# Kernel optimization log

Hardware: AMD Instinct MI355X
Metric: run time of the kernel (lower is better)

## Reference

```python
import jax, jax.numpy as jnp
import numpy as np

N = 1_500_000  # nodes (250k tracklets x 6 hits)
E = 12_000_000  # edges


def setup_inputs() -> dict:
    key = jax.random.key(0)
    ks = jax.random.split(key, 26)
    w = lambda k, shape: (jax.random.normal(k, shape, jnp.float32) * 0.1)
    inp = {
        "x": jax.random.normal(ks[0], (N, 1), jnp.float32),
        "edge_index": jax.random.randint(ks[1], (2, E), 0, N),
        "edge_attr": jax.random.normal(ks[2], (E, 2), jnp.float32),
        # conv1: in=1, prop=9, edge=2, out=9
        "Wx1": w(ks[3], (9, 1)), "bx1": w(ks[4], (9,)),
        "We1": w(ks[5], (9, 2)), "be1": w(ks[6], (9,)),
        "Wo1": w(ks[7], (9, 9)), "bo1": w(ks[8], (9,)),
        # conv2: in=9, prop=9, edge=2, out=9
        "Wx2": w(ks[9], (9, 9)), "bx2": w(ks[10], (9,)),
        "We2": w(ks[11], (9, 2)), "be2": w(ks[12], (9,)),
        "Wo2": w(ks[13], (9, 9)), "bo2": w(ks[14], (9,)),
        # conv3: in=9, prop=9, edge=2, out=4
        "Wx3": w(ks[15], (9, 9)), "bx3": w(ks[16], (9,)),
        "We3": w(ks[17], (9, 2)), "be3": w(ks[18], (9,)),
        "Wo3": w(ks[19], (4, 9)), "bo3": w(ks[20], (4,)),
        # head MLP
        "W1": w(ks[21], (8, 24)), "b1": w(ks[22], (8,)),
        "W2": w(ks[23], (4, 8)), "b2": w(ks[24], (4,)),
    }
    return inp


def _conv(x, src, dst, edge_attr, Wx, bx, We, be, Wo, bo):
    # trackletGNN: lin_x -> gather x_j -> * lin_edge(edge_attr) -> scatter-add -> lin_out
    h = x @ Wx.T + bx                      # [N, P]
    msg = h[src] * (edge_attr @ We.T + be)  # [E, P] gather + edge linear + multiply
    agg = jax.ops.segment_sum(msg, dst, num_segments=x.shape[0])  # [N, P]
    return agg @ Wo.T + bo


def reference(x, edge_index, edge_attr,
              Wx1, bx1, We1, be1, Wo1, bo1,
              Wx2, bx2, We2, be2, Wo2, bo2,
              Wx3, bx3, We3, be3, Wo3, bo3,
              W1, b1, W2, b2):
    src, dst = edge_index[0], edge_index[1]
    h = jax.nn.relu(_conv(x, src, dst, edge_attr, Wx1, bx1, We1, be1, Wo1, bo1))
    h = jax.nn.relu(_conv(h, src, dst, edge_attr, Wx2, bx2, We2, be2, Wo2, bo2))
    h = jax.nn.relu(_conv(h, src, dst, edge_attr, Wx3, bx3, We3, be3, Wo3, bo3))
    h = h.reshape(-1, 24)                   # 6 nodes x 4 feats per tracklet
    h = jax.nn.relu(h @ W1.T + b1)
    h = h @ W2.T + b2
    return jax.nn.log_softmax(h, axis=1)
```

## Files before the change

### kernel.cpp

```cpp
#include <hip/hip_runtime.h>
#include <hip/hip_bf16.h>


#define NNODES 1500000
#define NEDGES 12000000
#define NTRACK 250000
#define BSH    9
#define BSZ    512
#define BMASK  511u
#define NBUCK  2930
#define EGRID  1465
#define PCHUNK 4096
#define PBLK   2930
#define NSEG   32
#define SEGC   92
#define NTILE  46
#define SRCMASK 0x1FFFFFu
#define NSLICE 48
#define SRTR   10
#define FXSCALE 16777216.f
#define FXINV   (1.f / 16777216.f)

typedef unsigned int   u32;
typedef unsigned short u16;

static __device__ __forceinline__ float b2f(u32 v) {
    union { float f; u32 u; } x; x.u = v << 16; return x.f;
}
static __device__ __forceinline__ u16 f2b(float f) {
    __hip_bfloat16 h = __float2bfloat16(f);
    return *reinterpret_cast<u16*>(&h);
}
static __device__ __forceinline__ float ldw(const void* p, int i, int isf32) {
    return isf32 ? ((const float*)p)[i] : b2f((u32)((const u16*)p)[i]);
}
static __device__ __forceinline__ int fx(float f) {
    return (int)rintf(f * FXSCALE);
}


__global__ void k_detect(const u16* a, const u16* b, const u16* c,
                         const u16* d, const u16* e, const u16* f,
                         int* flag) {
    if (blockIdx.x == 0 && threadIdx.x == 0) {
        int isf32 = 0;
        const u16* ps[6] = {a, b, c, d, e, f};
        const int  ns[6] = {9, 9, 9, 9, 9, 8};
        for (int k = 0; k < 6; k++)
            for (int i = 0; i < ns[k]; i++) {
                float v = b2f((u32)ps[k][i]);
                if (!(fabsf(v) < 1.0e3f)) isf32 = 1;
            }
        *flag = isf32;
    }
}


__global__ __launch_bounds__(256) void k_xcast(const void* __restrict__ x,
                                               u16* __restrict__ xb,
                                               const int* __restrict__ flag) {
    int isf32 = *flag;
    int n = blockIdx.x * 256 + threadIdx.x;
    if (n < NNODES)
        xb[n] = isf32 ? f2b(((const float*)x)[n]) : ((const u16*)x)[n];
}


__global__ __launch_bounds__(512) void k_hist(const int* __restrict__ dst,
                                              u16* __restrict__ cnt) {
    __shared__ u32 h[NBUCK];
    int t = threadIdx.x;
    int chunk = blockIdx.x;
    int c0 = chunk * PCHUNK;
    for (int b = t; b < NBUCK; b += 512) h[b] = 0;
    __syncthreads();
#pragma unroll
    for (int k = 0; k < 8; k++) {
        int e = c0 + k * 512 + t;
        if (e < NEDGES) atomicAdd(&h[((u32)dst[e]) >> BSH], 1u);
    }
    __syncthreads();
    size_t row = (size_t)chunk * NBUCK;
    for (int b = t; b < NBUCK; b += 512) cnt[row + b] = (u16)h[b];
}


__global__ __launch_bounds__(64) void k_mscanA(const u16* __restrict__ cnt,
                                               u16* __restrict__ offm,
                                               u16* __restrict__ st) {
    int seg  = blockIdx.x / NTILE;
    int tile = blockIdx.x % NTILE;
    int b = tile * 64 + threadIdx.x;
    if (b >= NBUCK) return;
    int cS = seg * SEGC;
    int cE = cS + SEGC; if (cE > PBLK) cE = PBLK;
    u32 run = 0;
#pragma unroll 4
    for (int c = cS; c < cE; c++) {
        size_t idx = (size_t)c * NBUCK + b;
        u32 v = (u32)cnt[idx];
        offm[idx] = (u16)run;
        run += v;
    }
    st[(size_t)seg * NBUCK + b] = (u16)run;
}


__global__ __launch_bounds__(256) void k_mscanB(const u16* __restrict__ st,
                                                int* __restrict__ bstart,
                                                u32* __restrict__ segb) {
    __shared__ u32 sd[256];
    __shared__ u32 carry;
    int t = threadIdx.x;
    if (t == 0) carry = 0;
    __syncthreads();
    for (int c0 = 0; c0 < NBUCK; c0 += 256) {
        int b = c0 + t;
        u32 tot = 0;
        if (b < NBUCK)
#pragma unroll
            for (int s = 0; s < NSEG; s++) tot += (u32)st[(size_t)s * NBUCK + b];
        sd[t] = tot; __syncthreads();
        for (int o = 1; o < 256; o <<= 1) {
            u32 a = (t >= o) ? sd[t - o] : 0;
            __syncthreads();
            sd[t] += a;
            __syncthreads();
        }
        u32 excl = carry + sd[t] - tot;
        if (b < NBUCK) {
            bstart[b] = (int)excl;
            u32 r = excl;
#pragma unroll
            for (int s = 0; s < NSEG; s++) {
                segb[(size_t)s * NBUCK + b] = r;
                r += (u32)st[(size_t)s * NBUCK + b];
            }
        }
        __syncthreads();
        if (t == 255) carry += sd[255];
        __syncthreads();
    }
    if (t == 0) bstart[NBUCK] = NEDGES;
}


__global__ __launch_bounds__(512) void k_part(const int* __restrict__ src,
                                              const int* __restrict__ dst,
                                              const void* __restrict__ attr,
                                              const u16* __restrict__ cnt,
                                              const u16* __restrict__ offm,
                                              const u32* __restrict__ segb,
                                              uint2* __restrict__ perm,
                                              const int* __restrict__ flag) {
    __shared__ u32   cur[NBUCK];
    __shared__ u32   gbA[NBUCK];
    __shared__ uint2 rec[PCHUNK];
    __shared__ u16   bid[PCHUNK];
    __shared__ u32   wsum[8];
    __shared__ u32   carryS;
    int isf32 = *flag;
    int t = threadIdx.x;

    int bx = blockIdx.x & 7, bk = blockIdx.x >> 3;
    int chunk = ((bx < 2) ? bx * 367 : 2 * 367 + (bx - 2) * 366) + bk;

    int seg = chunk / SEGC;
    int c0 = chunk * PCHUNK;
    int chunkN = NEDGES - c0; if (chunkN > PCHUNK) chunkN = PCHUNK;
    size_t row = (size_t)chunk * NBUCK;

    for (int b = t; b < NBUCK; b += 512) cur[b] = (u32)cnt[row + b];
    if (t == 0) carryS = 0;
    __syncthreads();

    int lane = t & 63, wv = t >> 6;
    for (int b0 = 0; b0 < NBUCK; b0 += 512) {
        int b = b0 + t;
        u32 v = (b < NBUCK) ? cur[b] : 0;
        u32 xs = v;
#pragma unroll
        for (int o = 1; o < 64; o <<= 1) {
            u32 y = __shfl_up(xs, o, 64);
            if (lane >= o) xs += y;
        }
        if (lane == 63) wsum[wv] = xs;
        __syncthreads();
        if (t < 8) {
            u32 ws = wsum[t];
#pragma unroll
            for (int o = 1; o < 8; o <<= 1) {
                u32 y = __shfl_up(ws, o, 8);
                if (t >= o) ws += y;
            }
            wsum[t] = ws;
        }
        __syncthreads();
        u32 incl = xs + (wv ? wsum[wv - 1] : 0);
        if (b < NBUCK) cur[b] = carryS + incl - v;
        __syncthreads();
        if (t == 0) carryS += wsum[7];
        __syncthreads();
    }

    for (int b = t; b < NBUCK; b += 512)
        gbA[b] = segb[(size_t)seg * NBUCK + b] + (u32)offm[row + b] - cur[b];
    __syncthreads();

#pragma unroll
    for (int k = 0; k < 8; k++) {
        int e = c0 + k * 512 + t;
        if (e < NEDGES) {
            u32 d = (u32)dst[e];
            u32 s = (u32)src[e];
            u32 fb = d >> BSH;
            u32 ap;
            if (isf32) {
                float2 a = ((const float2*)attr)[e];
                ap = (u32)f2b(a.x) | ((u32)f2b(a.y) << 16);
            } else {
                ap = ((const u32*)attr)[e];
            }
            int slot = (int)atomicAdd(&cur[fb], 1u);
            uint2 r; r.x = s | ((d & BMASK) << 21); r.y = ap;
            rec[slot] = r;
            bid[slot] = (u16)fb;
        }
    }
    __syncthreads();

#pragma unroll
    for (int j = 0; j < 8; j++) {
        int s = j * 512 + t;
        if (s < chunkN) {
            u32 fb = (u32)bid[s];
            perm[gbA[fb] + s] = rec[s];
        }
    }
}


__global__ __launch_bounds__(512) void k_srt(const int* __restrict__ bstart,
                                             uint2* __restrict__ perm) {
    __shared__ int h[NSLICE];
    int t = threadIdx.x;
    int b = blockIdx.x;
    int r0 = bstart[b], r1 = bstart[b + 1];
    int len = r1 - r0;
    if (len <= 0) return;
    if (len > SRTR * 512) return;
    if (t < NSLICE) h[t] = 0;
    __syncthreads();

    uint2 r[SRTR];
#pragma unroll
    for (int k = 0; k < SRTR; k++) {
        int i = r0 + k * 512 + t;
        if (i < r1) {
            r[k] = perm[i];
            atomicAdd(&h[(r[k].x & SRCMASK) >> 15], 1);
        } else {
            r[k].x = 0xFFFFFFFFu;
        }
    }
    __syncthreads();

    if (t == 0) {
        int s = 0;
        for (int k = 0; k < NSLICE; k++) { int c = h[k]; h[k] = s; s += c; }
    }
    __syncthreads();

#pragma unroll
    for (int k = 0; k < SRTR; k++) {
        if (r[k].x != 0xFFFFFFFFu) {
            int slot = atomicAdd(&h[(r[k].x & SRCMASK) >> 15], 1);
            perm[r0 + slot] = r[k];
        }
    }
}


__global__ __launch_bounds__(256) void k_eagg1(
        const int* __restrict__ bstart, const uint2* __restrict__ perm,
        const u16* __restrict__ xb,
        const void* Wx, const void* bx, const void* We, const void* be,
        const void* Wo, const void* bo, const void* Wxn, const void* bxn,
        uint4* __restrict__ hA, u16* __restrict__ hB,
        const int* __restrict__ flag) {
    __shared__ int acc[BSZ * 9];
    __shared__ float sWx[9], sbx[9], sWe[18], sbe[9], sWo[81], sbo[9], sWxn[81], sbxn[9];
    int isf32 = *flag;
    int t = threadIdx.x;
    if (t < 9)  sWx[t]  = ldw(Wx,  t, isf32);
    if (t < 9)  sbx[t]  = ldw(bx,  t, isf32);
    if (t < 18) sWe[t]  = ldw(We,  t, isf32);
    if (t < 9)  sbe[t]  = ldw(be,  t, isf32);
    if (t < 81) sWo[t]  = ldw(Wo,  t, isf32);
    if (t < 9)  sbo[t]  = ldw(bo,  t, isf32);
    if (t < 81) sWxn[t] = ldw(Wxn, t, isf32);
    if (t < 9)  sbxn[t] = ldw(bxn, t, isf32);
    for (int i = t; i < BSZ * 9; i += 256) acc[i] = 0;
    __syncthreads();

    int b = blockIdx.x;
    int r0 = bstart[b], r1 = bstart[b + 1];
    for (int i = r0 + t; i < r1; i += 256) {
        uint2 rec = perm[i];
        int   l   = (int)((rec.x >> 21) & BMASK);
        float xs  = b2f((u32)xb[rec.x & SRCMASK]);
        float a0  = b2f(rec.y & 0xffffu);
        float a1  = b2f(rec.y >> 16);
        int* ap = &acc[l * 9];
#pragma unroll
        for (int j = 0; j < 9; j++) {
            float e  = fmaf(a0, sWe[2 * j], fmaf(a1, sWe[2 * j + 1], sbe[j]));
            float hh = fmaf(xs, sWx[j], sbx[j]);
            atomicAdd(&ap[j], fx(hh * e));
        }
    }
    __syncthreads();

    for (int l = t; l < BSZ; l += 256) {
        int n = b * BSZ + l;
        if (n >= NNODES) break;
        float av[9];
#pragma unroll
        for (int j = 0; j < 9; j++) av[j] = (float)acc[l * 9 + j] * FXINV;
        float o[9];
#pragma unroll
        for (int k = 0; k < 9; k++) {
            float v = sbo[k];
#pragma unroll
            for (int j = 0; j < 9; j++) v = fmaf(av[j], sWo[k * 9 + j], v);
            o[k] = fmaxf(v, 0.f);
        }
        u16 hv[9];
#pragma unroll
        for (int j = 0; j < 9; j++) {
            float v = sbxn[j];
#pragma unroll
            for (int k = 0; k < 9; k++) v = fmaf(o[k], sWxn[j * 9 + k], v);
            hv[j] = f2b(v);
        }
        uint4 q;
        q.x = (u32)hv[0] | ((u32)hv[1] << 16);
        q.y = (u32)hv[2] | ((u32)hv[3] << 16);
        q.z = (u32)hv[4] | ((u32)hv[5] << 16);
        q.w = (u32)hv[6] | ((u32)hv[7] << 16);
        hA[n] = q;
        hB[n] = hv[8];
    }
}


template <int OUTF, bool FUSE_NEXT>
__global__ __launch_bounds__(256) void k_eagg(
        const int* __restrict__ bstart, const uint2* __restrict__ perm,
        const uint4* __restrict__ hA, const u16* __restrict__ hB,
        const void* We, const void* be, const void* Wo, const void* bo,
        const void* Wxn, const void* bxn,
        uint4* __restrict__ oA, u16* __restrict__ oB,
        const int* __restrict__ flag) {
    __shared__ int acc[BSZ * 9];
    __shared__ float sWe[18], sbe[9], sWo[OUTF * 9], sbo[OUTF];
    __shared__ float sWxn[FUSE_NEXT ? 81 : 1], sbxn[FUSE_NEXT ? 9 : 1];
    int isf32 = *flag;
    int t = threadIdx.x;
    if (t < 18)       sWe[t] = ldw(We, t, isf32);
    if (t < 9)        sbe[t] = ldw(be, t, isf32);
    if (t < OUTF * 9) sWo[t] = ldw(Wo, t, isf32);
    if (t < OUTF)     sbo[t] = ldw(bo, t, isf32);
    if constexpr (FUSE_NEXT) {
        if (t < 81) sWxn[t] = ldw(Wxn, t, isf32);
        if (t < 9)  sbxn[t] = ldw(bxn, t, isf32);
    }
    __syncthreads();

#pragma unroll 1
    for (int half = 0; half < 2; half++) {
        int b = blockIdx.x * 2 + half;
        if (b >= NBUCK) break;

        for (int i = t; i < BSZ * 9; i += 256) acc[i] = 0;
        __syncthreads();

        int r0 = bstart[b], r1 = bstart[b + 1];
        for (int i = r0 + t; i < r1; i += 256) {
            uint2 rec = perm[i];
            int   s   = (int)(rec.x & SRCMASK);
            int   l   = (int)((rec.x >> 21) & BMASK);
            float a0  = b2f(rec.y & 0xffffu);
            float a1  = b2f(rec.y >> 16);
            uint4 qa  = hA[s];
            u32   qb  = (u32)hB[s];
            float ev[9];
#pragma unroll
            for (int j = 0; j < 9; j++)
                ev[j] = fmaf(a0, sWe[2 * j], fmaf(a1, sWe[2 * j + 1], sbe[j]));
            float h[9];
            h[0] = b2f(qa.x & 0xffffu); h[1] = b2f(qa.x >> 16);
            h[2] = b2f(qa.y & 0xffffu); h[3] = b2f(qa.y >> 16);
            h[4] = b2f(qa.z & 0xffffu); h[5] = b2f(qa.z >> 16);
            h[6] = b2f(qa.w & 0xffffu); h[7] = b2f(qa.w >> 16);
            h[8] = b2f(qb);
            int* ap = &acc[l * 9];
#pragma unroll
            for (int j = 0; j < 9; j++)
                atomicAdd(&ap[j], fx(h[j] * ev[j]));
        }
        __syncthreads();

        for (int l = t; l < BSZ; l += 256) {
            int n = b * BSZ + l;
            if (n >= NNODES) break;
            float av[9];
#pragma unroll
            for (int j = 0; j < 9; j++) av[j] = (float)acc[l * 9 + j] * FXINV;
            float o[OUTF];
#pragma unroll
            for (int k = 0; k < OUTF; k++) {
                float v = sbo[k];
#pragma unroll
                for (int j = 0; j < 9; j++) v = fmaf(av[j], sWo[k * 9 + j], v);
                o[k] = fmaxf(v, 0.f);
            }
            if constexpr (FUSE_NEXT) {
                u16 hv[9];
#pragma unroll
                for (int j = 0; j < 9; j++) {
                    float v = sbxn[j];
#pragma unroll
                    for (int k = 0; k < OUTF; k++) v = fmaf(o[k], sWxn[j * 9 + k], v);
                    hv[j] = f2b(v);
                }
                uint4 q;
                q.x = (u32)hv[0] | ((u32)hv[1] << 16);
                q.y = (u32)hv[2] | ((u32)hv[3] << 16);
                q.z = (u32)hv[4] | ((u32)hv[5] << 16);
                q.w = (u32)hv[6] | ((u32)hv[7] << 16);
                oA[n] = q;
                oB[n] = hv[8];
            } else {
                uint2 q;
                q.x = (u32)f2b(o[0]) | ((u32)f2b(o[1]) << 16);
                q.y = (u32)f2b(o[2]) | ((u32)f2b(o[3]) << 16);
                ((uint2*)oA)[n] = q;
            }
        }
        __syncthreads();
    }
}


__global__ __launch_bounds__(256) void k_head(
        const u16* __restrict__ f,
        const void* W1, const void* b1, const void* W2, const void* b2,
        void* __restrict__ out, const int* __restrict__ flag) {
    __shared__ float sW1[192], sb1[8], sW2[32], sb2[4];
    int isf32 = *flag;
    int t = threadIdx.x;
    if (t < 192) sW1[t] = ldw(W1, t, isf32);
    if (t < 8)   sb1[t] = ldw(b1, t, isf32);
    if (t < 32)  sW2[t] = ldw(W2, t, isf32);
    if (t < 4)   sb2[t] = ldw(b2, t, isf32);
    __syncthreads();

    int tr = blockIdx.x * 256 + t;
    if (tr >= NTRACK) return;

    const uint4* fp = (const uint4*)(f + (size_t)tr * 24);
    uint4 A = fp[0], B = fp[1], C = fp[2];
    u32 w[12] = {A.x, A.y, A.z, A.w, B.x, B.y, B.z, B.w, C.x, C.y, C.z, C.w};
    float in[24];
#pragma unroll
    for (int i = 0; i < 12; i++) {
        in[2 * i]     = b2f(w[i] & 0xffffu);
        in[2 * i + 1] = b2f(w[i] >> 16);
    }

    float z1[8];
#pragma unroll
    for (int o = 0; o < 8; o++) {
        float v = sb1[o];
#pragma unroll
        for (int i = 0; i < 24; i++) v = fmaf(in[i], sW1[o * 24 + i], v);
        z1[o] = fmaxf(v, 0.f);
    }
    float z2[4];
#pragma unroll
    for (int c = 0; c < 4; c++) {
        float v = sb2[c];
#pragma unroll
        for (int o = 0; o < 8; o++) v = fmaf(z1[o], sW2[c * 8 + o], v);
        z2[c] = v;
    }
    float m = fmaxf(fmaxf(z2[0], z2[1]), fmaxf(z2[2], z2[3]));
    float s = 0.f;
#pragma unroll
    for (int c = 0; c < 4; c++) s += expf(z2[c] - m);
    float l = logf(s) + m;

    if (isf32) {
        float4 q; q.x = z2[0] - l; q.y = z2[1] - l; q.z = z2[2] - l; q.w = z2[3] - l;
        ((float4*)((float*)out + (size_t)tr * 4))[0] = q;
    } else {
        uint2 q;
        q.x = (u32)f2b(z2[0] - l) | ((u32)f2b(z2[1] - l) << 16);
        q.y = (u32)f2b(z2[2] - l) | ((u32)f2b(z2[3] - l) << 16);
        ((uint2*)((u16*)out + (size_t)tr * 4))[0] = q;
    }
}


extern "C" void kernel_launch(void* const* d_in, const int* in_sizes, int n_in,
                              void* d_out, int out_size, void* d_ws, size_t ws_size,
                              hipStream_t stream) {
    const void* X    = d_in[0];
    const int* eidx  = (const int*)d_in[1];
    const void* eattr= d_in[2];
    const void *WX1 = d_in[3],  *BX1 = d_in[4];
    const void *WE1 = d_in[5],  *BE1 = d_in[6];
    const void *WO1 = d_in[7],  *BO1 = d_in[8];
    const void *WX2 = d_in[9],  *BX2 = d_in[10];
    const void *WE2 = d_in[11], *BE2 = d_in[12];
    const void *WO2 = d_in[13], *BO2 = d_in[14];
    const void *WX3 = d_in[15], *BX3 = d_in[16];
    const void *WE3 = d_in[17], *BE3 = d_in[18];
    const void *WO3 = d_in[19], *BO3 = d_in[20];
    const void *W1  = d_in[21], *B1  = d_in[22];
    const void *W2  = d_in[23], *B2  = d_in[24];

    const int* src = eidx;
    const int* dst = eidx + NEDGES;

    char* w = (char*)d_ws;
    size_t off = 0;
    auto take = [&](size_t bytes) -> void* {
        void* p = w + off;
        off += (bytes + 255) & ~(size_t)255;
        return p;
    };
    int*   flag   = (int*)take(256);
    int*   bstart = (int*)take((size_t)(NBUCK + 1) * 4);
    u16*   cnt    = (u16*)take((size_t)PBLK * NBUCK * 2);
    u16*   offm   = (u16*)take((size_t)PBLK * NBUCK * 2);
    u16*   st     = (u16*)take((size_t)NSEG * NBUCK * 2);
    u32*   segb   = (u32*)take((size_t)NSEG * NBUCK * 4);
    u16*   xb     = (u16*)take((size_t)NNODES * 2);
    uint2* perm   = (uint2*)take((size_t)NEDGES * 8);
    uint4* hA2    = (uint4*)take((size_t)NNODES * 16);
    u16*   hB2    = (u16*)take((size_t)NNODES * 2);
    uint4* hA3    = (uint4*)take((size_t)NNODES * 16);
    u16*   hB3    = (u16*)take((size_t)NNODES * 2);
    u16*   f      = (u16*)hA2;
    (void)ws_size; (void)n_in; (void)in_sizes; (void)out_size;

    const int NB = (NNODES + 255) / 256;
    const int TB = (NTRACK + 255) / 256;

    k_detect <<<1,    64,  0, stream>>>((const u16*)BX1, (const u16*)BE1, (const u16*)BO1,
                                        (const u16*)BX2, (const u16*)BE2, (const u16*)B1, flag);
    k_xcast  <<<NB,   256, 0, stream>>>(X, xb, flag);
    k_hist   <<<PBLK, 512, 0, stream>>>(dst, cnt);
    k_mscanA <<<NSEG * NTILE, 64, 0, stream>>>(cnt, offm, st);
    k_mscanB <<<1,    256, 0, stream>>>(st, bstart, segb);
    k_part   <<<PBLK, 512, 0, stream>>>(src, dst, eattr, cnt, offm, segb, perm, flag);
    k_srt    <<<NBUCK,512, 0, stream>>>(bstart, perm);

    k_eagg1        <<<NBUCK, 256, 0, stream>>>(bstart, perm, xb,
                                               WX1, BX1, WE1, BE1, WO1, BO1, WX2, BX2,
                                               hA2, hB2, flag);
    k_eagg<9,true> <<<EGRID, 256, 0, stream>>>(bstart, perm, hA2, hB2,
                                               WE2, BE2, WO2, BO2, WX3, BX3,
                                               hA3, hB3, flag);
    k_eagg<4,false><<<EGRID, 256, 0, stream>>>(bstart, perm, hA3, hB3,
                                               WE3, BE3, WO3, BO3, WO3, BO3,
                                               (uint4*)f, (u16*)f, flag);
    k_head         <<<TB,    256, 0, stream>>>(f, W1, B1, W2, B2, d_out, flag);
}
```

Measured before the change: 953.0 us.

## Fuse bucket sort into first edge-aggregation kernel and use nontemporal memory ops

Merges the per-bucket source-slice sort kernel with the first convolution's edge aggregation, so the records held in registers after sorting feed the layer-1 aggregation directly. This removes one full read of the permuted edge array and one kernel launch. Separately, streaming loads and stores of edges and node features are marked nontemporal to reduce cache pollution. The fused kernel runs at 512 threads per block with more register pressure, and aggregation order in layer 1 now follows the unsorted register order, which is harmless because accumulation is fixed-point.

```diff
diff --git a/kernel.cpp b/kernel.cpp
--- a/kernel.cpp
+++ b/kernel.cpp
@@ -23,6 +23,8 @@
 
 typedef unsigned int   u32;
 typedef unsigned short u16;
+typedef u32 v2u __attribute__((ext_vector_type(2)));
+typedef u32 v4u __attribute__((ext_vector_type(4)));
 
 static __device__ __forceinline__ float b2f(u32 v) {
     union { float f; u32 u; } x; x.u = v << 16; return x.f;
@@ -36,6 +38,34 @@
 }
 static __device__ __forceinline__ int fx(float f) {
     return (int)rintf(f * FXSCALE);
+}
+static __device__ __forceinline__ uint2 ntld2(const uint2* p) {
+    v2u v = __builtin_nontemporal_load((const v2u*)p);
+    uint2 r; r.x = v.x; r.y = v.y; return r;
+}
+static __device__ __forceinline__ int ntldi(const int* p) {
+    return __builtin_nontemporal_load(p);
+}
+static __device__ __forceinline__ u32 ntldu(const u32* p) {
+    return __builtin_nontemporal_load(p);
+}
+static __device__ __forceinline__ float2 ntldf2(const float2* p) {
+    v2u v = __builtin_nontemporal_load((const v2u*)p);
+    float2 r;
+    union { float f; u32 u; } a, b;
+    a.u = v.x; b.u = v.y; r.x = a.f; r.y = b.f;
+    return r;
+}
+static __device__ __forceinline__ void ntst4(uint4* p, uint4 q) {
+    v4u v; v.x = q.x; v.y = q.y; v.z = q.z; v.w = q.w;
+    __builtin_nontemporal_store(v, (v4u*)p);
+}
+static __device__ __forceinline__ void ntst2(uint2* p, uint2 q) {
+    v2u v; v.x = q.x; v.y = q.y;
+    __builtin_nontemporal_store(v, (v2u*)p);
+}
+static __device__ __forceinline__ void ntstw(u16* p, u16 q) {
+    __builtin_nontemporal_store(q, p);
 }
 
 
@@ -77,7 +107,7 @@
 #pragma unroll
     for (int k = 0; k < 8; k++) {
         int e = c0 + k * 512 + t;
-        if (e < NEDGES) atomicAdd(&h[((u32)dst[e]) >> BSH], 1u);
+        if (e < NEDGES) atomicAdd(&h[((u32)ntldi(&dst[e])) >> BSH], 1u);
     }
     __syncthreads();
     size_t row = (size_t)chunk * NBUCK;
@@ -211,15 +241,15 @@
     for (int k = 0; k < 8; k++) {
         int e = c0 + k * 512 + t;
         if (e < NEDGES) {
-            u32 d = (u32)dst[e];
-            u32 s = (u32)src[e];
+            u32 d = (u32)ntldi(&dst[e]);
+            u32 s = (u32)ntldi(&src[e]);
             u32 fb = d >> BSH;
             u32 ap;
             if (isf32) {
-                float2 a = ((const float2*)attr)[e];
+                float2 a = ntldf2(&((const float2*)attr)[e]);
                 ap = (u32)f2b(a.x) | ((u32)f2b(a.y) << 16);
             } else {
-                ap = ((const u32*)attr)[e];
+                ap = ntldu(&((const u32*)attr)[e]);
             }
             int slot = (int)atomicAdd(&cur[fb], 1u);
             uint2 r; r.x = s | ((d & BMASK) << 21); r.y = ap;
@@ -240,55 +270,15 @@
 }
 
 
-__global__ __launch_bounds__(512) void k_srt(const int* __restrict__ bstart,
-                                             uint2* __restrict__ perm) {
-    __shared__ int h[NSLICE];
-    int t = threadIdx.x;
-    int b = blockIdx.x;
-    int r0 = bstart[b], r1 = bstart[b + 1];
-    int len = r1 - r0;
-    if (len <= 0) return;
-    if (len > SRTR * 512) return;
-    if (t < NSLICE) h[t] = 0;
-    __syncthreads();
-
-    uint2 r[SRTR];
-#pragma unroll
-    for (int k = 0; k < SRTR; k++) {
-        int i = r0 + k * 512 + t;
-        if (i < r1) {
-            r[k] = perm[i];
-            atomicAdd(&h[(r[k].x & SRCMASK) >> 15], 1);
-        } else {
-            r[k].x = 0xFFFFFFFFu;
-        }
-    }
-    __syncthreads();
-
-    if (t == 0) {
-        int s = 0;
-        for (int k = 0; k < NSLICE; k++) { int c = h[k]; h[k] = s; s += c; }
-    }
-    __syncthreads();
-
-#pragma unroll
-    for (int k = 0; k < SRTR; k++) {
-        if (r[k].x != 0xFFFFFFFFu) {
-            int slot = atomicAdd(&h[(r[k].x & SRCMASK) >> 15], 1);
-            perm[r0 + slot] = r[k];
-        }
-    }
-}
-
-
-__global__ __launch_bounds__(256) void k_eagg1(
-        const int* __restrict__ bstart, const uint2* __restrict__ perm,
+__global__ __launch_bounds__(512) void k_srtagg1(
+        const int* __restrict__ bstart, uint2* __restrict__ perm,
         const u16* __restrict__ xb,
         const void* Wx, const void* bx, const void* We, const void* be,
         const void* Wo, const void* bo, const void* Wxn, const void* bxn,
         uint4* __restrict__ hA, u16* __restrict__ hB,
         const int* __restrict__ flag) {
     __shared__ int acc[BSZ * 9];
+    __shared__ int h[NSLICE];
     __shared__ float sWx[9], sbx[9], sWe[18], sbe[9], sWo[81], sbo[9], sWxn[81], sbxn[9];
     int isf32 = *flag;
     int t = threadIdx.x;
@@ -300,56 +290,104 @@
     if (t < 9)  sbo[t]  = ldw(bo,  t, isf32);
     if (t < 81) sWxn[t] = ldw(Wxn, t, isf32);
     if (t < 9)  sbxn[t] = ldw(bxn, t, isf32);
-    for (int i = t; i < BSZ * 9; i += 256) acc[i] = 0;
+    if (t < NSLICE) h[t] = 0;
+    for (int i = t; i < BSZ * 9; i += 512) acc[i] = 0;
     __syncthreads();
 
     int b = blockIdx.x;
     int r0 = bstart[b], r1 = bstart[b + 1];
-    for (int i = r0 + t; i < r1; i += 256) {
-        uint2 rec = perm[i];
-        int   l   = (int)((rec.x >> 21) & BMASK);
-        float xs  = b2f((u32)xb[rec.x & SRCMASK]);
-        float a0  = b2f(rec.y & 0xffffu);
-        float a1  = b2f(rec.y >> 16);
-        int* ap = &acc[l * 9];
-#pragma unroll
-        for (int j = 0; j < 9; j++) {
-            float e  = fmaf(a0, sWe[2 * j], fmaf(a1, sWe[2 * j + 1], sbe[j]));
-            float hh = fmaf(xs, sWx[j], sbx[j]);
-            atomicAdd(&ap[j], fx(hh * e));
-        }
-    }
-    __syncthreads();
-
-    for (int l = t; l < BSZ; l += 256) {
+    int len = r1 - r0;
+
+    if (len > 0 && len <= SRTR * 512) {
+        uint2 r[SRTR];
+#pragma unroll
+        for (int k = 0; k < SRTR; k++) {
+            int i = r0 + k * 512 + t;
+            if (i < r1) {
+                r[k] = ntld2(&perm[i]);
+                atomicAdd(&h[(r[k].x & SRCMASK) >> 15], 1);
+            } else {
+                r[k].x = 0xFFFFFFFFu;
+            }
+        }
+        __syncthreads();
+        if (t == 0) {
+            int s = 0;
+            for (int k = 0; k < NSLICE; k++) { int c = h[k]; h[k] = s; s += c; }
+        }
+        __syncthreads();
+#pragma unroll
+        for (int k = 0; k < SRTR; k++) {
+            if (r[k].x != 0xFFFFFFFFu) {
+                int slot = atomicAdd(&h[(r[k].x & SRCMASK) >> 15], 1);
+                perm[r0 + slot] = r[k];
+            }
+        }
+#pragma unroll
+        for (int k = 0; k < SRTR; k++) {
+            if (r[k].x != 0xFFFFFFFFu) {
+                int   l  = (int)((r[k].x >> 21) & BMASK);
+                float xs = b2f((u32)xb[r[k].x & SRCMASK]);
+                float a0 = b2f(r[k].y & 0xffffu);
+                float a1 = b2f(r[k].y >> 16);
+                int* ap = &acc[l * 9];
+#pragma unroll
+                for (int j = 0; j < 9; j++) {
+                    float e  = fmaf(a0, sWe[2 * j], fmaf(a1, sWe[2 * j + 1], sbe[j]));
+                    float hh = fmaf(xs, sWx[j], sbx[j]);
+                    atomicAdd(&ap[j], fx(hh * e));
+                }
+            }
+        }
+    } else if (len > 0) {
+        for (int i = r0 + t; i < r1; i += 512) {
+            uint2 rec = perm[i];
+            int   l  = (int)((rec.x >> 21) & BMASK);
+            float xs = b2f((u32)xb[rec.x & SRCMASK]);
+            float a0 = b2f(rec.y & 0xffffu);
+            float a1 = b2f(rec.y >> 16);
+            int* ap = &acc[l * 9];
+#pragma unroll
+            for (int j = 0; j < 9; j++) {
+                float e  = fmaf(a0, sWe[2 * j], fmaf(a1, sWe[2 * j + 1], sbe[j]));
+                float hh = fmaf(xs, sWx[j], sbx[j]);
+                atomicAdd(&ap[j], fx(hh * e));
+            }
+        }
+    }
+    __syncthreads();
+
+    int l = t;
+    if (l < BSZ) {
         int n = b * BSZ + l;
-        if (n >= NNODES) break;
-        float av[9];
-#pragma unroll
-        for (int j = 0; j < 9; j++) av[j] = (float)acc[l * 9 + j] * FXINV;
-        float o[9];
-#pragma unroll
-        for (int k = 0; k < 9; k++) {
-            float v = sbo[k];
-#pragma unroll
-            for (int j = 0; j < 9; j++) v = fmaf(av[j], sWo[k * 9 + j], v);
-            o[k] = fmaxf(v, 0.f);
-        }
-        u16 hv[9];
-#pragma unroll
-        for (int j = 0; j < 9; j++) {
-            float v = sbxn[j];
-#pragma unroll
-            for (int k = 0; k < 9; k++) v = fmaf(o[k], sWxn[j * 9 + k], v);
-            hv[j] = f2b(v);
-        }
-        uint4 q;
-        q.x = (u32)hv[0] | ((u32)hv[1] << 16);
-        q.y = (u32)hv[2] | ((u32)hv[3] << 16);
-        q.z = (u32)hv[4] | ((u32)hv[5] << 16);
-        q.w = (u32)hv[6] | ((u32)hv[7] << 16);
-        hA[n] = q;
-        hB[n] = hv[8];
+        if (n < NNODES) {
+            float av[9];
+#pragma unroll
+            for (int j = 0; j < 9; j++) av[j] = (float)acc[l * 9 + j] * FXINV;
+            float o[9];
+#pragma unroll
+            for (int k = 0; k < 9; k++) {
+                float v = sbo[k];
+#pragma unroll
+                for (int j = 0; j < 9; j++) v = fmaf(av[j], sWo[k * 9 + j], v);
+                o[k] = fmaxf(v, 0.f);
+            }
+            u16 hv[9];
+#pragma unroll
+            for (int j = 0; j < 9; j++) {
+                float v = sbxn[j];
+#pragma unroll
+                for (int k = 0; k < 9; k++) v = fmaf(o[k], sWxn[j * 9 + k], v);
+                hv[j] = f2b(v);
+            }
+            uint4 q;
+            q.x = (u32)hv[0] | ((u32)hv[1] << 16);
+            q.y = (u32)hv[2] | ((u32)hv[3] << 16);
+            q.z = (u32)hv[4] | ((u32)hv[5] << 16);
+            q.w = (u32)hv[6] | ((u32)hv[7] << 16);
+            ntst4(&hA[n], q);
+            ntstw(&hB[n], hv[8]);
+        }
     }
 }
 
@@ -387,7 +425,7 @@
 
         int r0 = bstart[b], r1 = bstart[b + 1];
         for (int i = r0 + t; i < r1; i += 256) {
-            uint2 rec = perm[i];
+            uint2 rec = ntld2(&perm[i]);
             int   s   = (int)(rec.x & SRCMASK);
             int   l   = (int)((rec.x >> 21) & BMASK);
             float a0  = b2f(rec.y & 0xffffu);
@@ -439,13 +477,13 @@
                 q.y = (u32)hv[2] | ((u32)hv[3] << 16);
                 q.z = (u32)hv[4] | ((u32)hv[5] << 16);
                 q.w = (u32)hv[6] | ((u32)hv[7] << 16);
-                oA[n] = q;
-                oB[n] = hv[8];
+                ntst4(&oA[n], q);
+                ntstw(&oB[n], hv[8]);
             } else {
                 uint2 q;
                 q.x = (u32)f2b(o[0]) | ((u32)f2b(o[1]) << 16);
                 q.y = (u32)f2b(o[2]) | ((u32)f2b(o[3]) << 16);
-                ((uint2*)oA)[n] = q;
+                ntst2(&((uint2*)oA)[n], q);
             }
         }
         __syncthreads();
@@ -566,9 +604,8 @@
     k_mscanA <<<NSEG * NTILE, 64, 0, stream>>>(cnt, offm, st);
     k_mscanB <<<1,    256, 0, stream>>>(st, bstart, segb);
     k_part   <<<PBLK, 512, 0, stream>>>(src, dst, eattr, cnt, offm, segb, perm, flag);
-    k_srt    <<<NBUCK,512, 0, stream>>>(bstart, perm);
-
-    k_eagg1        <<<NBUCK, 256, 0, stream>>>(bstart, perm, xb,
+
+    k_srtagg1      <<<NBUCK, 512, 0, stream>>>(bstart, perm, xb,
                                                WX1, BX1, WE1, BE1, WO1, BO1, WX2, BX2,
                                                hA2, hB2, flag);
     k_eagg<9,true> <<<EGRID, 256, 0, stream>>>(bstart, perm, hA2, hB2,
```

Result: faster. 901.3 us (-5.4%).
